# Optimization experiments

Hardware: AMD Instinct MI355X
Metric: run time of the kernel (lower is better)

## Reference

```python
import jax, jax.numpy as jnp
import numpy as np

# --- configuration matching setup_inputs ---
N_EVENTS = 4          # number of events in the ragged batch (row_splits has 5 entries)
HITS_PER_EVENT = 50000
K_CLUSTERS = 256      # max truth shower index per event
Q_MIN = 1.0
REPULSION_CONTRIB = 0.5
SCALE = 1.0
EPS = 1e-6


def setup_inputs() -> dict:
    key = jax.random.key(0)
    k1, k2 = jax.random.split(key)
    n = N_EVENTS * HITS_PER_EVENT
    coords = jax.random.normal(k1, (n, 3), dtype=jnp.float32)
    truth_indices = jax.random.randint(k2, (n, 1), 0, K_CLUSTERS, dtype=jnp.int32)
    row_splits = (jnp.arange(N_EVENTS + 1, dtype=jnp.int32) * HITS_PER_EVENT)
    return {"coords": coords, "truth_indices": truth_indices, "row_splits": row_splits}


def _oc_cluster_loss(coords, truth_indices):
    """Object-condensation attractive/repulsive potentials.

    coords:        [n, C] float clustering coordinates (n = E * Nev, equal splits)
    truth_indices: [n, 1] int cluster id per hit, in [0, K)
    Returns (V_att, V_rep) scalars, averaged over events.
    """
    C = coords.shape[1]
    x = coords.reshape(N_EVENTS, HITS_PER_EVENT, C)            # [E, N, C]
    t = truth_indices.reshape(N_EVENTS, HITS_PER_EVENT)        # [E, N]

    # beta_like = 0.5 (3-input path of LLClusterCoordinates) -> constant charge
    beta = jnp.float32(0.5)
    q_val = jnp.arctanh(beta) ** 2 + jnp.float32(Q_MIN)        # scalar
    q = jnp.full((N_EVENTS, HITS_PER_EVENT), q_val, dtype=coords.dtype)  # [E, N]

    # membership mask (one-hot over truth clusters)
    M = jax.nn.one_hot(t, K_CLUSTERS, dtype=coords.dtype)      # [E, N, K]
    qM = M * q[..., None]                                      # [E, N, K]

    # q-weighted average condensation point per cluster (use_average_cc_pos=True)
    sum_q = jnp.sum(qM, axis=1)                                # [E, K]
    x_cc = jnp.einsum('enk,enc->ekc', qM, x) / (sum_q[..., None] + EPS)  # [E, K, C]

    # charge of the condensation (max-beta) vertex per cluster
    q_alpha = jnp.max(qM, axis=1)                              # [E, K] (0 for empty clusters)

    # pairwise hit <-> condensation-point distances
    diff = x[:, :, None, :] - x_cc[:, None, :, :]              # [E, N, K, C]
    d2 = jnp.sum(diff * diff, axis=-1)                         # [E, N, K]
    d = jnp.sqrt(d2 + EPS)

    w = q[..., None] * q_alpha[:, None, :]                     # [E, N, K]
    n_per_ev = jnp.float32(HITS_PER_EVENT)

    V_att_ev = jnp.sum(M * w * d2, axis=(1, 2)) / n_per_ev                   # [E]
    V_rep_ev = jnp.sum((1.0 - M) * w * jax.nn.relu(1.0 - d), axis=(1, 2)) / n_per_ev
    return jnp.mean(V_att_ev), jnp.mean(V_rep_ev)


def reference(coords, truth_indices, row_splits):
    V_att, V_rep = _oc_cluster_loss(coords, truth_indices)
    lossval = SCALE * ((1.0 - REPULSION_CONTRIB) * V_att + REPULSION_CONTRIB * V_rep)
    # layer returns (inputs[0], lossval) when return_lossval=True
    return coords, lossval
```

## Files before the change

kernel.cpp:

```cpp
#include <hip/hip_runtime.h>

typedef float v2f __attribute__((ext_vector_type(2)));

#define E_EVENTS 4
#define NPE 50000
#define K_CL 256
#define QV 1.30173724f
#define EPSF 1e-6f
#define SB 64
#define BPE 196
#define HALFK 128
#define LOSS_SCALE 2.5e-6f
#define LOSS_IDX (3 * E_EVENTS * NPE)

__global__ __launch_bounds__(256) void k_sums(const float* __restrict__ coords,
                                              const int* __restrict__ truth,
                                              float* __restrict__ partial) {
    __shared__ float s[4 * K_CL];
    int tid = threadIdx.x;
    #pragma unroll
    for (int i = 0; i < 4; ++i) s[tid + 256 * i] = 0.0f;
    __syncthreads();

    int e = blockIdx.x >> 6, blk = blockIdx.x & (SB - 1);
    for (int local = blk * 256 + tid; local < NPE; local += SB * 256) {
        int h = e * NPE + local;
        int t = truth[h];
        float x = coords[3 * h], y = coords[3 * h + 1], z = coords[3 * h + 2];
        atomicAdd(&s[t], x);
        atomicAdd(&s[K_CL + t], y);
        atomicAdd(&s[2 * K_CL + t], z);
        atomicAdd(&s[3 * K_CL + t], 1.0f);
    }
    __syncthreads();

    float* g = partial + blockIdx.x * 1024;
    #pragma unroll
    for (int i = 0; i < 4; ++i) g[tid + 256 * i] = s[tid + 256 * i];
}

__global__ __launch_bounds__(64) void k_cc(const float* __restrict__ partial,
                                           float4* __restrict__ cc,
                                           float* __restrict__ out) {
    int gid = blockIdx.x * 64 + threadIdx.x;
    int e = gid >> 8, k = gid & (K_CL - 1);
    float sx = 0.f, sy = 0.f, sz = 0.f, cn = 0.f;
    const float* base = partial + e * SB * 1024 + k;
    #pragma unroll 4
    for (int b = 0; b < SB; ++b) {
        const float* p = base + b * 1024;
        sx += p[0]; sy += p[256]; sz += p[512]; cn += p[768];
    }
    float inv = QV / (QV * cn + EPSF);
    float qa = (cn > 0.0f) ? QV : 0.0f;
    cc[gid] = make_float4(sx * inv, sy * inv, sz * inv, qa);
    if (gid == 0) out[LOSS_IDX] = 0.0f;
}

__global__ __launch_bounds__(256) void k_main(const float* __restrict__ coords,
                                              const int* __restrict__ truth,
                                              const float4* __restrict__ cc,
                                              float* __restrict__ out) {
    __shared__ v2f sxv[HALFK / 2], syv[HALFK / 2], szv[HALFK / 2], swv[HALFK / 2];
    int tid = threadIdx.x;
    int b = blockIdx.x;
    int e = b / (2 * BPE);
    int r = b - e * (2 * BPE);
    int hh = r / BPE;
    int blk = r - hh * BPE;
    if (tid < HALFK) {
        float4 c = cc[e * K_CL + hh * HALFK + tid];
        ((float*)sxv)[tid] = c.x; ((float*)syv)[tid] = c.y;
        ((float*)szv)[tid] = c.z; ((float*)swv)[tid] = c.w;
    }
    __syncthreads();

    int local = blk * 256 + tid;
    float contrib = 0.0f;
    if (local < NPE) {
        int h = e * NPE + local;
        float x = coords[3 * h], y = coords[3 * h + 1], z = coords[3 * h + 2];
        int t = truth[h];
        if (hh == 0) {
            out[3 * h] = x; out[3 * h + 1] = y; out[3 * h + 2] = z;
        }

        const v2f ONE = {1.0f, 1.0f}, ZER = {0.0f, 0.0f}, EPS2 = {EPSF, EPSF};
        v2f X = {x, x}, Y = {y, y}, Z = {z, z};
        v2f rep = {0.0f, 0.0f};
        #pragma unroll 8
        for (int k2 = 0; k2 < HALFK / 2; ++k2) {
            v2f dx = X - sxv[k2], dy = Y - syv[k2], dz = Z - szv[k2];
            v2f d2 = __builtin_elementwise_fma(dx, dx,
                     __builtin_elementwise_fma(dy, dy,
                     __builtin_elementwise_fma(dz, dz, EPS2)));
            v2f d = {__builtin_amdgcn_sqrtf(d2.x), __builtin_amdgcn_sqrtf(d2.y)};
            v2f rr = __builtin_elementwise_max(ONE - d, ZER);
            rep = __builtin_elementwise_fma(swv[k2], rr, rep);
        }
        contrib = QV * (rep.x + rep.y);

        if ((t >> 7) == hh) {
            int tl = t & (HALFK - 1);
            float cx = ((float*)sxv)[tl], cy = ((float*)syv)[tl];
            float cz = ((float*)szv)[tl], cw = ((float*)swv)[tl];
            float dx = x - cx, dy = y - cy, dz = z - cz;
            float d2o = fmaf(dx, dx, fmaf(dy, dy, dz * dz));
            float dno = __builtin_amdgcn_sqrtf(d2o + EPSF);
            contrib += QV * fmaf(QV, d2o, -cw * fmaxf(0.0f, 1.0f - dno));
        }
    }

    #pragma unroll
    for (int o = 32; o > 0; o >>= 1) contrib += __shfl_down(contrib, o, 64);
    __shared__ float wsum[4];
    if ((tid & 63) == 0) wsum[tid >> 6] = contrib;
    __syncthreads();
    if (tid == 0) {
        float bsum = wsum[0] + wsum[1] + wsum[2] + wsum[3];
        atomicAdd(out + LOSS_IDX, bsum * LOSS_SCALE);
    }
}

extern "C" void kernel_launch(void* const* d_in, const int* in_sizes, int n_in,
                              void* d_out, int out_size, void* d_ws, size_t ws_size,
                              hipStream_t stream) {
    const float* coords = (const float*)d_in[0];
    const int*   truth  = (const int*)d_in[1];

    float*  partial = (float*)d_ws;
    float4* cc      = (float4*)((char*)d_ws + (1 << 20));
    float*  out     = (float*)d_out;

    k_sums<<<E_EVENTS * SB, 256, 0, stream>>>(coords, truth, partial);
    k_cc  <<<16, 64, 0, stream>>>(partial, cc, out);
    k_main<<<E_EVENTS * 2 * BPE, 256, 0, stream>>>(coords, truth, cc, out);
}
```

Measured before the change: 98.74 us.

## Prune repulsion work to hits near condensation points via compacted list

The single main kernel is split into an attractive/pass-through kernel and a repulsion kernel. The centroid kernel now computes, per event, the largest centroid norm and a radius bound `1 + max|c|`. Hits outside that radius cannot be within distance 1 of any centroid, so only hits inside it are compacted into a per-event list with ballot-based atomics. Only those hits go through the all-cluster repulsion loop, which now uses an expanded |x|^2 - 2x·c + |c|^2 form with precomputed centroid norms. This trades an extra launch, the list writes and a gather against skipping the sqrt loop for most hits. The skip is exact by the triangle inequality for any input, though the expanded distance form can lose some floating-point precision.

```diff
diff --git a/kernel.cpp b/kernel.cpp
--- a/kernel.cpp
+++ b/kernel.cpp
@@ -1,15 +1,16 @@
 #include <hip/hip_runtime.h>
 
-typedef float v2f __attribute__((ext_vector_type(2)));
+typedef unsigned long long ull;
 
 #define E_EVENTS 4
 #define NPE 50000
 #define K_CL 256
 #define QV 1.30173724f
+#define QV2 (QV * QV)
 #define EPSF 1e-6f
 #define SB 64
 #define BPE 196
-#define HALFK 128
+#define RB 64
 #define LOSS_SCALE 2.5e-6f
 #define LOSS_IDX (3 * E_EVENTS * NPE)
 
@@ -26,10 +27,9 @@
     for (int local = blk * 256 + tid; local < NPE; local += SB * 256) {
         int h = e * NPE + local;
         int t = truth[h];
-        float x = coords[3 * h], y = coords[3 * h + 1], z = coords[3 * h + 2];
-        atomicAdd(&s[t], x);
-        atomicAdd(&s[K_CL + t], y);
-        atomicAdd(&s[2 * K_CL + t], z);
+        atomicAdd(&s[t],            coords[3 * h]);
+        atomicAdd(&s[K_CL + t],     coords[3 * h + 1]);
+        atomicAdd(&s[2 * K_CL + t], coords[3 * h + 2]);
         atomicAdd(&s[3 * K_CL + t], 1.0f);
     }
     __syncthreads();
@@ -39,11 +39,12 @@
     for (int i = 0; i < 4; ++i) g[tid + 256 * i] = s[tid + 256 * i];
 }
 
-__global__ __launch_bounds__(64) void k_cc(const float* __restrict__ partial,
-                                           float4* __restrict__ cc,
-                                           float* __restrict__ out) {
-    int gid = blockIdx.x * 64 + threadIdx.x;
-    int e = gid >> 8, k = gid & (K_CL - 1);
+__global__ __launch_bounds__(256) void k_cc(const float* __restrict__ partial,
+                                            float4* __restrict__ cc,
+                                            float* __restrict__ thresh2,
+                                            int* __restrict__ counter,
+                                            float* __restrict__ out) {
+    int e = blockIdx.x, k = threadIdx.x;
     float sx = 0.f, sy = 0.f, sz = 0.f, cn = 0.f;
     const float* base = partial + e * SB * 1024 + k;
     #pragma unroll 4
@@ -52,62 +53,66 @@
         sx += p[0]; sy += p[256]; sz += p[512]; cn += p[768];
     }
     float inv = QV / (QV * cn + EPSF);
-    float qa = (cn > 0.0f) ? QV : 0.0f;
-    cc[gid] = make_float4(sx * inv, sy * inv, sz * inv, qa);
-    if (gid == 0) out[LOSS_IDX] = 0.0f;
+    float cx = sx * inv, cy = sy * inv, cz = sz * inv;
+    float ccn = fmaf(cx, cx, fmaf(cy, cy, cz * cz));
+    bool empty = (cn == 0.0f);
+    cc[e * K_CL + k] = empty ? make_float4(0.f, 0.f, 0.f, 1e9f)
+                             : make_float4(cx, cy, cz, ccn);
+
+    float nrm = empty ? 0.f : __builtin_amdgcn_sqrtf(ccn);
+    #pragma unroll
+    for (int o = 32; o > 0; o >>= 1) nrm = fmaxf(nrm, __shfl_down(nrm, o, 64));
+    __shared__ float wmax[4];
+    if ((k & 63) == 0) wmax[k >> 6] = nrm;
+    __syncthreads();
+    if (k == 0) {
+        float M = fmaxf(fmaxf(wmax[0], wmax[1]), fmaxf(wmax[2], wmax[3]));
+        float th = 1.0f + M + 1e-3f;
+        thresh2[e] = th * th;
+        counter[e] = 0;
+        if (e == 0) out[LOSS_IDX] = 0.0f;
+    }
 }
 
-__global__ __launch_bounds__(256) void k_main(const float* __restrict__ coords,
-                                              const int* __restrict__ truth,
-                                              const float4* __restrict__ cc,
-                                              float* __restrict__ out) {
-    __shared__ v2f sxv[HALFK / 2], syv[HALFK / 2], szv[HALFK / 2], swv[HALFK / 2];
+__global__ __launch_bounds__(256) void k_att(const float* __restrict__ coords,
+                                             const int* __restrict__ truth,
+                                             const float4* __restrict__ cc,
+                                             const float* __restrict__ thresh2,
+                                             int* __restrict__ counter,
+                                             int* __restrict__ list,
+                                             float* __restrict__ out) {
     int tid = threadIdx.x;
-    int b = blockIdx.x;
-    int e = b / (2 * BPE);
-    int r = b - e * (2 * BPE);
-    int hh = r / BPE;
-    int blk = r - hh * BPE;
-    if (tid < HALFK) {
-        float4 c = cc[e * K_CL + hh * HALFK + tid];
-        ((float*)sxv)[tid] = c.x; ((float*)syv)[tid] = c.y;
-        ((float*)szv)[tid] = c.z; ((float*)swv)[tid] = c.w;
-    }
-    __syncthreads();
+    int e = blockIdx.x / BPE;
+    int local = (blockIdx.x - e * BPE) * 256 + tid;
+    bool valid = local < NPE;
 
-    int local = blk * 256 + tid;
-    float contrib = 0.0f;
-    if (local < NPE) {
+    float contrib = 0.0f, pp = 1e30f;
+    if (valid) {
         int h = e * NPE + local;
         float x = coords[3 * h], y = coords[3 * h + 1], z = coords[3 * h + 2];
         int t = truth[h];
-        if (hh == 0) {
-            out[3 * h] = x; out[3 * h + 1] = y; out[3 * h + 2] = z;
-        }
+        out[3 * h] = x; out[3 * h + 1] = y; out[3 * h + 2] = z;
 
-        const v2f ONE = {1.0f, 1.0f}, ZER = {0.0f, 0.0f}, EPS2 = {EPSF, EPSF};
-        v2f X = {x, x}, Y = {y, y}, Z = {z, z};
-        v2f rep = {0.0f, 0.0f};
-        #pragma unroll 8
-        for (int k2 = 0; k2 < HALFK / 2; ++k2) {
-            v2f dx = X - sxv[k2], dy = Y - syv[k2], dz = Z - szv[k2];
-            v2f d2 = __builtin_elementwise_fma(dx, dx,
-                     __builtin_elementwise_fma(dy, dy,
-                     __builtin_elementwise_fma(dz, dz, EPS2)));
-            v2f d = {__builtin_amdgcn_sqrtf(d2.x), __builtin_amdgcn_sqrtf(d2.y)};
-            v2f rr = __builtin_elementwise_max(ONE - d, ZER);
-            rep = __builtin_elementwise_fma(swv[k2], rr, rep);
-        }
-        contrib = QV * (rep.x + rep.y);
+        float4 c = cc[e * K_CL + t];
+        float dx = x - c.x, dy = y - c.y, dz = z - c.z;
+        float d2o = fmaf(dx, dx, fmaf(dy, dy, dz * dz));
+        float dno = __builtin_amdgcn_sqrtf(d2o + EPSF);
+        contrib = QV2 * (d2o - fmaxf(0.0f, 1.0f - dno));
+        pp = fmaf(x, x, fmaf(y, y, z * z));
+    }
 
-        if ((t >> 7) == hh) {
-            int tl = t & (HALFK - 1);
-            float cx = ((float*)sxv)[tl], cy = ((float*)syv)[tl];
-            float cz = ((float*)szv)[tl], cw = ((float*)swv)[tl];
-            float dx = x - cx, dy = y - cy, dz = z - cz;
-            float d2o = fmaf(dx, dx, fmaf(dy, dy, dz * dz));
-            float dno = __builtin_amdgcn_sqrtf(d2o + EPSF);
-            contrib += QV * fmaf(QV, d2o, -cw * fmaxf(0.0f, 1.0f - dno));
+    bool inner = valid && (pp < thresh2[e]);
+    ull mask = __ballot(inner);
+    int cnt = __popcll(mask);
+    if (cnt > 0) {
+        int lane = tid & 63;
+        int leader = __ffsll(mask) - 1;
+        int base = 0;
+        if (lane == leader) base = atomicAdd(&counter[e], cnt);
+        base = __shfl(base, leader, 64);
+        if (inner) {
+            int prefix = __popcll(mask & ((1ull << lane) - 1ull));
+            list[e * NPE + base + prefix] = local;
         }
     }
 
@@ -116,10 +121,53 @@
     __shared__ float wsum[4];
     if ((tid & 63) == 0) wsum[tid >> 6] = contrib;
     __syncthreads();
-    if (tid == 0) {
-        float bsum = wsum[0] + wsum[1] + wsum[2] + wsum[3];
-        atomicAdd(out + LOSS_IDX, bsum * LOSS_SCALE);
+    if (tid == 0)
+        atomicAdd(out + LOSS_IDX,
+                  (wsum[0] + wsum[1] + wsum[2] + wsum[3]) * LOSS_SCALE);
+}
+
+__global__ __launch_bounds__(256) void k_rep(const float* __restrict__ coords,
+                                             const float4* __restrict__ cc,
+                                             const int* __restrict__ counter,
+                                             const int* __restrict__ list,
+                                             float* __restrict__ out) {
+    __shared__ float4 scc[K_CL / 2];
+    int tid = threadIdx.x;
+    int b = blockIdx.x;
+    int e = b / (2 * RB);
+    int r = b - e * (2 * RB);
+    int hh = r / RB;
+    int rb = r - hh * RB;
+    if (tid < K_CL / 2) scc[tid] = cc[e * K_CL + hh * (K_CL / 2) + tid];
+    __syncthreads();
+
+    int n = counter[e];
+    float rsum = 0.0f;
+    for (int idx = rb * 256 + tid; idx < n; idx += RB * 256) {
+        int h = e * NPE + list[e * NPE + idx];
+        float x = coords[3 * h], y = coords[3 * h + 1], z = coords[3 * h + 2];
+        float m2x = -2.0f * x, m2y = -2.0f * y, m2z = -2.0f * z;
+        float ppe = fmaf(x, x, fmaf(y, y, fmaf(z, z, EPSF)));
+        float rep = 0.0f;
+        #pragma unroll 16
+        for (int k = 0; k < K_CL / 2; ++k) {
+            float4 c = scc[k];
+            float d2 = fmaf(m2x, c.x, fmaf(m2y, c.y, fmaf(m2z, c.z, c.w))) + ppe;
+            float d = __builtin_amdgcn_sqrtf(d2);
+            rep += fmaxf(0.0f, 1.0f - d);
+        }
+        rsum += rep;
     }
+    float contrib = QV2 * rsum;
+
+    #pragma unroll
+    for (int o = 32; o > 0; o >>= 1) contrib += __shfl_down(contrib, o, 64);
+    __shared__ float wsum[4];
+    if ((tid & 63) == 0) wsum[tid >> 6] = contrib;
+    __syncthreads();
+    if (tid == 0)
+        atomicAdd(out + LOSS_IDX,
+                  (wsum[0] + wsum[1] + wsum[2] + wsum[3]) * LOSS_SCALE);
 }
 
 extern "C" void kernel_launch(void* const* d_in, const int* in_sizes, int n_in,
@@ -128,11 +176,17 @@
     const float* coords = (const float*)d_in[0];
     const int*   truth  = (const int*)d_in[1];
 
-    float*  partial = (float*)d_ws;
-    float4* cc      = (float4*)((char*)d_ws + (1 << 20));
+    char* ws = (char*)d_ws;
+    float*  partial = (float*)ws;
+    float4* cc      = (float4*)(ws + (1 << 20));
+    float*  thresh2 = (float*)(ws + (1 << 20) + 16384);
+    int*    counter = (int*)(ws + (1 << 20) + 16384 + 64);
+    int*    list    = (int*)(ws + (1 << 20) + 16384 + 128);
     float*  out     = (float*)d_out;
 
     k_sums<<<E_EVENTS * SB, 256, 0, stream>>>(coords, truth, partial);
-    k_cc  <<<16, 64, 0, stream>>>(partial, cc, out);
-    k_main<<<E_EVENTS * 2 * BPE, 256, 0, stream>>>(coords, truth, cc, out);
+    k_cc  <<<E_EVENTS, 256, 0, stream>>>(partial, cc, thresh2, counter, out);
+    k_att <<<E_EVENTS * BPE, 256, 0, stream>>>(coords, truth, cc, thresh2,
+                                               counter, list, out);
+    k_rep <<<E_EVENTS * 2 * RB, 256, 0, stream>>>(coords, cc, counter, list, out);
 }
```

After: 125.2 us. 1.27x slower.
